# Optimization experiments

Hardware: AMD Instinct MI355X
Metric: run time of the kernel (lower is better)

Reference implementation:

```python
import jax, jax.numpy as jnp
import numpy as np

N = 8192
INPUT_DIM = 3000
HIDDEN_DIM = 512
LATENT_DIM = 30
AVG_DEGREE = 32


def setup_inputs() -> dict:
    key = jax.random.key(0)
    k_x, k_g, k_w0, k_v0, k_v1, k_w1 = jax.random.split(key, 6)

    node_features = jax.random.normal(k_x, (N, INPUT_DIM), dtype=jnp.float32)

    # Binary adjacency, avg degree ~AVG_DEGREE, with self-loops so every
    # softmax row has at least one entry (mirrors typical spatial graphs).
    p = AVG_DEGREE / N
    adj = (jax.random.uniform(k_g, (N, N)) < p).astype(jnp.float32)
    idx = jnp.arange(N)
    graph = adj.at[idx, idx].set(1.0)

    def xavier(k, shape):
        fan_in, fan_out = shape
        limit = float(np.sqrt(6.0 / (fan_in + fan_out)))
        return jax.random.uniform(k, shape, jnp.float32, -limit, limit)

    W0 = xavier(k_w0, (INPUT_DIM, HIDDEN_DIM))
    v0 = xavier(k_v0, (HIDDEN_DIM, 1))
    v1 = xavier(k_v1, (HIDDEN_DIM, 1))
    W1 = xavier(k_w1, (HIDDEN_DIM, LATENT_DIM))

    return {"node_features": node_features, "graph": graph,
            "W0": W0, "v0": v0, "v1": v1, "W1": W1}


def _gat_layer(X_in, graph, W, v0, v1):
    # Projection
    X = X_in @ W                                   # [N, D]
    # Rank-1 pairwise scores, masked by adjacency
    f0 = X @ v0                                    # [N, 1]
    f1 = X @ v1                                    # [N, 1]
    E = graph * (f0 + f1.T)                        # [N, N]
    scores = jax.nn.sigmoid(E) - 0.5               # values kept by to_sparse
    mask = graph != 0
    # Masked softmax over dim=1 (torch.sparse.softmax over nnz of each row;
    # rows with no edges stay all-zero after to_dense)
    neg = jnp.finfo(scores.dtype).min
    w = jnp.where(mask, scores, neg)
    m = jnp.max(w, axis=1, keepdims=True)
    e = jnp.where(mask, jnp.exp(w - m), 0.0)
    s = jnp.sum(e, axis=1, keepdims=True)
    alphas = e / jnp.maximum(s, jnp.asarray(1e-30, scores.dtype))
    # Weighted aggregation + ELU
    return jax.nn.elu(alphas @ X)


def reference(node_features, graph, W0, v0, v1, W1):
    Z = _gat_layer(node_features, graph, W0, v0, v1)  # layer 0 (attention)
    Z = Z @ W1                                        # last layer: proj only
    return Z
```

## Files before the change

### kernel.cpp

```cpp
#include <hip/hip_runtime.h>
#include <stdint.h>

#define NN   8192
#define KDIM 3000
#define KP   3072
#define DDIM 512
#define LDIM 30

typedef __attribute__((ext_vector_type(8))) short short8;
typedef __attribute__((ext_vector_type(4))) float float4v;
typedef __attribute__((ext_vector_type(4))) float f4v;

__device__ __forceinline__ float bf2f(unsigned short h) {
    union { unsigned int u; float f; } v; v.u = ((unsigned int)h) << 16; return v.f;
}
__device__ __forceinline__ unsigned short f2bf(float f) {
    union { float f; unsigned int u; } v; v.f = f;
    unsigned int r = v.u + 0x7FFF + ((v.u >> 16) & 1);
    return (unsigned short)(r >> 16);
}
__device__ __forceinline__ void gl_lds16(const void* g, void* l) {
    __builtin_amdgcn_global_load_lds(
        (const __attribute__((address_space(1))) unsigned int*)g,
        (__attribute__((address_space(3))) unsigned int*)l, 16, 0, 0);
}

__global__ __launch_bounds__(384) void k_prep(
    const float* __restrict__ A, unsigned short* __restrict__ Abf,
    const float* __restrict__ W0, unsigned short* __restrict__ W0T,
    float* __restrict__ f01) {
    int bid = blockIdx.x, t = threadIdx.x;
    if (bid < NN) {
        int k = t * 8;
        uint4 o = {0, 0, 0, 0};
        if (k < KDIM) {
            const float* src = A + (size_t)bid * KDIM + k;
            float4 a = *(const float4*)src;
            float4 b = *(const float4*)(src + 4);
            unsigned short* h = (unsigned short*)&o;
            h[0] = f2bf(a.x); h[1] = f2bf(a.y); h[2] = f2bf(a.z); h[3] = f2bf(a.w);
            h[4] = f2bf(b.x); h[5] = f2bf(b.y); h[6] = f2bf(b.z); h[7] = f2bf(b.w);
        }
        *(uint4*)(Abf + (size_t)bid * KP + k) = o;
    } else if (bid < NN + 1536) {
        __shared__ float tile[32][33];
        int b = bid - NN;
        int k0 = (b % 96) * 32, n0 = (b / 96) * 32;
        int tx = t & 31, ty = (t >> 5) & 7;
        if (t < 256) {
            #pragma unroll
            for (int p = 0; p < 4; p++) {
                int k = k0 + ty + p * 8;
                float val = 0.f;
                if (k < KDIM) val = W0[(size_t)k * DDIM + n0 + tx];
                tile[ty + p * 8][tx] = val;
            }
        }
        __syncthreads();
        if (t < 256) {
            #pragma unroll
            for (int p = 0; p < 4; p++) {
                int k = k0 + tx;
                int n = n0 + ty + p * 8;
                W0T[(size_t)n * KP + k] = f2bf(tile[tx][ty + p * 8]);
            }
        }
    } else {
        for (int idx = t; idx < 2 * NN / 4; idx += 384)
            ((uint4*)f01)[idx] = (uint4){0, 0, 0, 0};
    }
}

#define BM 128
#define BN 64

__global__ __launch_bounds__(256) void k_gemm(
    const unsigned short* __restrict__ A,
    const unsigned short* __restrict__ BT,
    const float* __restrict__ v0,
    const float* __restrict__ v1,
    unsigned short* __restrict__ Xbf,
    float* __restrict__ f0,
    float* __restrict__ f1)
{
    __shared__ __align__(16) unsigned short As[2][BM][32];
    __shared__ __align__(16) unsigned short Bs[2][BN][32];
    int t = threadIdx.x, w = t >> 6, l = t & 63;
    int m0 = blockIdx.x * BM, n0 = blockIdx.y * BN;
    int wm = (w & 1) * 64, wn = (w >> 1) * 32;

    float4v acc[4][2];
    #pragma unroll
    for (int mf = 0; mf < 4; mf++)
        #pragma unroll
        for (int nf = 0; nf < 2; nf++)
            acc[mf][nf] = (float4v){0.f, 0.f, 0.f, 0.f};

    int lr = l >> 2;
    int lk = (l & 3) * 8;
    const unsigned short* Abase = A  + (size_t)m0 * KP;
    const unsigned short* Bbase = BT + (size_t)n0 * KP;
    const int lA = l & 15;
    const int qA = (l >> 4) * 8;

    for (int k0 = 0; k0 < KP; k0 += 64) {
        if (k0) __syncthreads();
        #pragma unroll
        for (int p = 0; p < 4; p++) {
            int q = w * 4 + p, h = q >> 3, rb = q & 7;
            gl_lds16(Abase + (size_t)(rb * 16 + lr) * KP + k0 + h * 32 + lk,
                     &As[h][rb * 16][0]);
        }
        #pragma unroll
        for (int p = 0; p < 2; p++) {
            int q = w * 2 + p, h = q >> 2, rb = q & 3;
            gl_lds16(Bbase + (size_t)(rb * 16 + lr) * KP + k0 + h * 32 + lk,
                     &Bs[h][rb * 16][0]);
        }
        __syncthreads();

        #pragma unroll
        for (int h = 0; h < 2; h++) {
            short8 af[4], bfr[2];
            #pragma unroll
            for (int mf = 0; mf < 4; mf++)
                af[mf] = *(const short8*)&As[h][wm + mf * 16 + lA][qA];
            #pragma unroll
            for (int nf = 0; nf < 2; nf++)
                bfr[nf] = *(const short8*)&Bs[h][wn + nf * 16 + lA][qA];
            #pragma unroll
            for (int mf = 0; mf < 4; mf++)
                #pragma unroll
                for (int nf = 0; nf < 2; nf++)
                    acc[mf][nf] = __builtin_amdgcn_mfma_f32_16x16x32_bf16(
                        af[mf], bfr[nf], acc[mf][nf], 0, 0, 0);
        }
    }

    int rq = (l >> 4) * 4;
    float vc0 = v0[n0 + wn + lA], vc1 = v0[n0 + wn + 16 + lA];
    float uc0 = v1[n0 + wn + lA], uc1 = v1[n0 + wn + 16 + lA];
    #pragma unroll
    for (int mf = 0; mf < 4; mf++) {
        #pragma unroll
        for (int nf = 0; nf < 2; nf++) {
            int col = n0 + wn + nf * 16 + lA;
            int row = m0 + wm + mf * 16 + rq;
            #pragma unroll
            for (int r = 0; r < 4; r++)
                Xbf[(size_t)(row + r) * DDIM + col] = f2bf(acc[mf][nf][r]);
        }
        #pragma unroll
        for (int r = 0; r < 4; r++) {
            float s0 = acc[mf][0][r] * vc0 + acc[mf][1][r] * vc1;
            float s1 = acc[mf][0][r] * uc0 + acc[mf][1][r] * uc1;
            #pragma unroll
            for (int off = 8; off; off >>= 1) {
                s0 += __shfl_xor(s0, off);
                s1 += __shfl_xor(s1, off);
            }
            if (lA == 0) {
                int row = m0 + wm + mf * 16 + rq + r;
                atomicAdd(&f0[row], s0);
                atomicAdd(&f1[row], s1);
            }
        }
    }
}

#define CAP 1024
__global__ __launch_bounds__(256) void k_aggregate(
    const float* __restrict__ G,
    const unsigned short* __restrict__ Xbf,
    const float* __restrict__ f0,
    const float* __restrict__ f1,
    const float* __restrict__ W1,
    float* __restrict__ out)
{
    __shared__ int cnt;
    __shared__ int   jlist[CAP];
    __shared__ float elist[CAP];
    __shared__ float zrow[DDIM];
    __shared__ float red[256];
    int t = threadIdx.x;
    int i = blockIdx.x;
    if (t == 0) cnt = 0;
    __syncthreads();

    float f0i = f0[i];
    const float* grow = G + (size_t)i * NN;
    #pragma unroll
    for (int it = 0; it < 8; it++) {
        int base = (it * 256 + t) * 4;
        f4v gv = __builtin_nontemporal_load((const f4v*)(grow + base));
        #pragma unroll
        for (int m = 0; m < 4; m++) {
            if (gv[m] != 0.f) {
                int j = base + m;
                float xe = f0i + f1[j];
                float sg = 1.0f / (1.0f + __expf(-xe));
                float e  = __expf(sg - 0.5f);
                int p = atomicAdd(&cnt, 1);
                if (p < CAP) { jlist[p] = j; elist[p] = e; }
            }
        }
    }
    __syncthreads();

    int n = cnt < CAP ? cnt : CAP;
    float s = 0.f;
    for (int k = 0; k < n; k++) s += elist[k];
    float inv = 1.0f / fmaxf(s, 1e-30f);

    float a0 = 0.f, a1 = 0.f;
    int k = 0;
    for (; k + 4 <= n; k += 4) {
        int j0 = jlist[k], j1 = jlist[k+1], j2 = jlist[k+2], j3 = jlist[k+3];
        float e0 = elist[k], e1 = elist[k+1], e2 = elist[k+2], e3 = elist[k+3];
        unsigned int x0 = *(const unsigned int*)(Xbf + (size_t)j0 * DDIM + t * 2);
        unsigned int x1 = *(const unsigned int*)(Xbf + (size_t)j1 * DDIM + t * 2);
        unsigned int x2 = *(const unsigned int*)(Xbf + (size_t)j2 * DDIM + t * 2);
        unsigned int x3 = *(const unsigned int*)(Xbf + (size_t)j3 * DDIM + t * 2);
        a0 += e0 * bf2f((unsigned short)(x0 & 0xFFFFu))
            + e1 * bf2f((unsigned short)(x1 & 0xFFFFu))
            + e2 * bf2f((unsigned short)(x2 & 0xFFFFu))
            + e3 * bf2f((unsigned short)(x3 & 0xFFFFu));
        a1 += e0 * bf2f((unsigned short)(x0 >> 16))
            + e1 * bf2f((unsigned short)(x1 >> 16))
            + e2 * bf2f((unsigned short)(x2 >> 16))
            + e3 * bf2f((unsigned short)(x3 >> 16));
    }
    for (; k < n; k++) {
        int j = jlist[k];
        float e = elist[k];
        unsigned int xw = *(const unsigned int*)(Xbf + (size_t)j * DDIM + t * 2);
        a0 += e * bf2f((unsigned short)(xw & 0xFFFFu));
        a1 += e * bf2f((unsigned short)(xw >> 16));
    }
    a0 *= inv; a1 *= inv;
    zrow[2 * t]     = a0 > 0.f ? a0 : __expf(a0) - 1.0f;
    zrow[2 * t + 1] = a1 > 0.f ? a1 : __expf(a1) - 1.0f;
    __syncthreads();

    int c = t & 31, slab = t >> 5;
    float p = 0.f;
    if (c < LDIM) {
        #pragma unroll 4
        for (int q = 0; q < 64; q++) {
            int d = slab * 64 + q;
            p += zrow[d] * W1[d * LDIM + c];
        }
    }
    red[t] = p;
    __syncthreads();
    if (t < LDIM) {
        float sum = 0.f;
        #pragma unroll
        for (int s2 = 0; s2 < 8; s2++) sum += red[s2 * 32 + t];
        out[(size_t)i * LDIM + t] = sum;
    }
}

extern "C" void kernel_launch(void* const* d_in, const int* in_sizes, int n_in,
                              void* d_out, int out_size, void* d_ws, size_t ws_size,
                              hipStream_t stream) {
    (void)in_sizes; (void)n_in; (void)out_size; (void)ws_size;
    const float* nf = (const float*)d_in[0];
    const float* G  = (const float*)d_in[1];
    const float* W0 = (const float*)d_in[2];
    const float* v0 = (const float*)d_in[3];
    const float* v1 = (const float*)d_in[4];
    const float* W1 = (const float*)d_in[5];
    float* out = (float*)d_out;

    char* ws = (char*)d_ws;
    size_t off = 0;
    unsigned short* Abf = (unsigned short*)(ws + off); off += (size_t)NN * KP * 2;
    unsigned short* W0T = (unsigned short*)(ws + off); off += (size_t)DDIM * KP * 2;
    unsigned short* Xbf = (unsigned short*)(ws + off); off += (size_t)NN * DDIM * 2;
    float* f0 = (float*)(ws + off); off += NN * 4;
    float* f1 = (float*)(ws + off); off += NN * 4;

    hipLaunchKernelGGL(k_prep, dim3(NN + 1536 + 1), dim3(384), 0, stream,
                       nf, Abf, W0, W0T, f0);
    hipLaunchKernelGGL(k_gemm, dim3(64, 8), dim3(256), 0, stream,
                       Abf, W0T, v0, v1, Xbf, f0, f1);
    hipLaunchKernelGGL(k_aggregate, dim3(NN), dim3(256), 0, stream,
                       G, Xbf, f0, f1, W1, out);
}
```

Baseline: 508.6 us.

## Overlap adjacency scan with projection GEMM by merging into one launch

Moves the dense adjacency-row scan (256 MB read) out of the aggregation kernel and into extra blocks of the GEMM launch, writing compact per-row neighbor lists to workspace. The bandwidth-bound scan can then run concurrently with the compute-bound GEMM, and the final kernel only reads small index lists. It also switches the prep-kernel feature loads to nontemporal loads. The neighbor cap drops from 1024 to 128 per row, which holds for average degree 32 but could silently truncate high-degree rows.

```diff
diff --git a/kernel.cpp b/kernel.cpp
--- a/kernel.cpp
+++ b/kernel.cpp
@@ -6,6 +6,8 @@
 #define KP   3072
 #define DDIM 512
 #define LDIM 30
+#define CAPJ 128
+#define GEMM_BLOCKS 512
 
 typedef __attribute__((ext_vector_type(8))) short short8;
 typedef __attribute__((ext_vector_type(4))) float float4v;
@@ -35,11 +37,11 @@
         uint4 o = {0, 0, 0, 0};
         if (k < KDIM) {
             const float* src = A + (size_t)bid * KDIM + k;
-            float4 a = *(const float4*)src;
-            float4 b = *(const float4*)(src + 4);
+            f4v a = __builtin_nontemporal_load((const f4v*)src);
+            f4v b = __builtin_nontemporal_load((const f4v*)(src + 4));
             unsigned short* h = (unsigned short*)&o;
-            h[0] = f2bf(a.x); h[1] = f2bf(a.y); h[2] = f2bf(a.z); h[3] = f2bf(a.w);
-            h[4] = f2bf(b.x); h[5] = f2bf(b.y); h[6] = f2bf(b.z); h[7] = f2bf(b.w);
+            h[0] = f2bf(a[0]); h[1] = f2bf(a[1]); h[2] = f2bf(a[2]); h[3] = f2bf(a[3]);
+            h[4] = f2bf(b[0]); h[5] = f2bf(b[1]); h[6] = f2bf(b[2]); h[7] = f2bf(b[3]);
         }
         *(uint4*)(Abf + (size_t)bid * KP + k) = o;
     } else if (bid < NN + 1536) {
@@ -74,19 +76,50 @@
 #define BM 128
 #define BN 64
 
-__global__ __launch_bounds__(256) void k_gemm(
+__global__ __launch_bounds__(256) void k_mid(
     const unsigned short* __restrict__ A,
     const unsigned short* __restrict__ BT,
     const float* __restrict__ v0,
     const float* __restrict__ v1,
     unsigned short* __restrict__ Xbf,
     float* __restrict__ f0,
-    float* __restrict__ f1)
+    float* __restrict__ f1,
+    const float* __restrict__ G,
+    int* __restrict__ jcnt,
+    int* __restrict__ jlist)
 {
     __shared__ __align__(16) unsigned short As[2][BM][32];
     __shared__ __align__(16) unsigned short Bs[2][BN][32];
+    __shared__ int scnt;
+    __shared__ int jbuf[CAPJ];
     int t = threadIdx.x, w = t >> 6, l = t & 63;
-    int m0 = blockIdx.x * BM, n0 = blockIdx.y * BN;
+    int bid = blockIdx.x;
+
+    if (bid >= GEMM_BLOCKS) {
+        int r = bid - GEMM_BLOCKS;
+        if (t == 0) scnt = 0;
+        __syncthreads();
+        const float* grow = G + (size_t)r * NN;
+        #pragma unroll
+        for (int it = 0; it < 8; it++) {
+            int base = (it * 256 + t) * 4;
+            f4v gv = __builtin_nontemporal_load((const f4v*)(grow + base));
+            #pragma unroll
+            for (int m = 0; m < 4; m++) {
+                if (gv[m] != 0.f) {
+                    int p = atomicAdd(&scnt, 1);
+                    if (p < CAPJ) jbuf[p] = base + m;
+                }
+            }
+        }
+        __syncthreads();
+        int n = scnt < CAPJ ? scnt : CAPJ;
+        if (t == 0) jcnt[r] = n;
+        if (t < n) jlist[(size_t)r * CAPJ + t] = jbuf[t];
+        return;
+    }
+
+    int m0 = (bid >> 3) * BM, n0 = (bid & 7) * BN;
     int wm = (w & 1) * 64, wn = (w >> 1) * 32;
 
     float4v acc[4][2];
@@ -168,46 +201,33 @@
     }
 }
 
-#define CAP 1024
-__global__ __launch_bounds__(256) void k_aggregate(
-    const float* __restrict__ G,
+__global__ __launch_bounds__(256) void k_final(
+    const int* __restrict__ jcnt,
+    const int* __restrict__ jlist,
     const unsigned short* __restrict__ Xbf,
     const float* __restrict__ f0,
     const float* __restrict__ f1,
     const float* __restrict__ W1,
     float* __restrict__ out)
 {
-    __shared__ int cnt;
-    __shared__ int   jlist[CAP];
-    __shared__ float elist[CAP];
+    __shared__ int   jloc[CAPJ];
+    __shared__ float elist[CAPJ];
     __shared__ float zrow[DDIM];
     __shared__ float red[256];
     int t = threadIdx.x;
     int i = blockIdx.x;
-    if (t == 0) cnt = 0;
+
+    int n = jcnt[i];
+    float f0i = f0[i];
+    if (t < n) {
+        int j = jlist[(size_t)i * CAPJ + t];
+        jloc[t] = j;
+        float xe = f0i + f1[j];
+        float sg = 1.0f / (1.0f + __expf(-xe));
+        elist[t] = __expf(sg - 0.5f);
+    }
     __syncthreads();
 
-    float f0i = f0[i];
-    const float* grow = G + (size_t)i * NN;
-    #pragma unroll
-    for (int it = 0; it < 8; it++) {
-        int base = (it * 256 + t) * 4;
-        f4v gv = __builtin_nontemporal_load((const f4v*)(grow + base));
-        #pragma unroll
-        for (int m = 0; m < 4; m++) {
-            if (gv[m] != 0.f) {
-                int j = base + m;
-                float xe = f0i + f1[j];
-                float sg = 1.0f / (1.0f + __expf(-xe));
-                float e  = __expf(sg - 0.5f);
-                int p = atomicAdd(&cnt, 1);
-                if (p < CAP) { jlist[p] = j; elist[p] = e; }
-            }
-        }
-    }
-    __syncthreads();
-
-    int n = cnt < CAP ? cnt : CAP;
     float s = 0.f;
     for (int k = 0; k < n; k++) s += elist[k];
     float inv = 1.0f / fmaxf(s, 1e-30f);
@@ -215,7 +235,7 @@
     float a0 = 0.f, a1 = 0.f;
     int k = 0;
     for (; k + 4 <= n; k += 4) {
-        int j0 = jlist[k], j1 = jlist[k+1], j2 = jlist[k+2], j3 = jlist[k+3];
+        int j0 = jloc[k], j1 = jloc[k+1], j2 = jloc[k+2], j3 = jloc[k+3];
         float e0 = elist[k], e1 = elist[k+1], e2 = elist[k+2], e3 = elist[k+3];
         unsigned int x0 = *(const unsigned int*)(Xbf + (size_t)j0 * DDIM + t * 2);
         unsigned int x1 = *(const unsigned int*)(Xbf + (size_t)j1 * DDIM + t * 2);
@@ -231,7 +251,7 @@
             + e3 * bf2f((unsigned short)(x3 >> 16));
     }
     for (; k < n; k++) {
-        int j = jlist[k];
+        int j = jloc[k];
         float e = elist[k];
         unsigned int xw = *(const unsigned int*)(Xbf + (size_t)j * DDIM + t * 2);
         a0 += e * bf2f((unsigned short)(xw & 0xFFFFu));
@@ -280,11 +300,13 @@
     unsigned short* Xbf = (unsigned short*)(ws + off); off += (size_t)NN * DDIM * 2;
     float* f0 = (float*)(ws + off); off += NN * 4;
     float* f1 = (float*)(ws + off); off += NN * 4;
+    int* jcnt  = (int*)(ws + off); off += NN * 4;
+    int* jlist = (int*)(ws + off); off += (size_t)NN * CAPJ * 4;
 
     hipLaunchKernelGGL(k_prep, dim3(NN + 1536 + 1), dim3(384), 0, stream,
                        nf, Abf, W0, W0T, f0);
-    hipLaunchKernelGGL(k_gemm, dim3(64, 8), dim3(256), 0, stream,
-                       Abf, W0T, v0, v1, Xbf, f0, f1);
-    hipLaunchKernelGGL(k_aggregate, dim3(NN), dim3(256), 0, stream,
-                       G, Xbf, f0, f1, W1, out);
-}
+    hipLaunchKernelGGL(k_mid, dim3(GEMM_BLOCKS + NN), dim3(256), 0, stream,
+                       Abf, W0T, v0, v1, Xbf, f0, f1, G, jcnt, jlist);
+    hipLaunchKernelGGL(k_final, dim3(NN), dim3(256), 0, stream,
+                       jcnt, jlist, Xbf, f0, f1, W1, out);
+}
```

After: 513.7 us. Within noise of the previous version (+1.0%).
